# Performance work log

Measured on AMD Instinct MI355X. Metric: run time of the kernel, lower is better.

Reference implementation:

```python
import jax, jax.numpy as jnp
import numpy as np

NUM_SLOTS = 8
SLOT_DIM = 64
HIDDEN_DIM = 128  # max(slot_dim, 128)
ITERS = 3
EPS = 1e-08
LN_EPS = 1e-05


def _ln(x, w, b):
    mu = jnp.mean(x, axis=-1, keepdims=True)
    var = jnp.mean(jnp.square(x - mu), axis=-1, keepdims=True)
    return (x - mu) * jax.lax.rsqrt(var + LN_EPS) * w + b


def setup_inputs() -> dict:
    key = jax.random.key(0)
    ks = jax.random.split(key, 16)
    b, n, d, h, n_s = 64, 4096, SLOT_DIM, HIDDEN_DIM, NUM_SLOTS
    s = 1.0 / np.sqrt(d)
    sh = 1.0 / np.sqrt(h)
    inp = {
        'inputs': jax.random.normal(ks[0], (b, n, d), jnp.float32),
        'mask': jax.random.randint(ks[1], (b, n), 0, 2, jnp.int32),
        'noise': jax.random.normal(ks[2], (b, n_s, d), jnp.float32),
        'slots_mu': jax.random.normal(ks[3], (1, 1, d), jnp.float32),
        'slots_sigma': jax.random.uniform(ks[4], (1, 1, d), jnp.float32),
        'Wq': jax.random.normal(ks[5], (d, d), jnp.float32) * s,
        'bq': jnp.zeros((d,), jnp.float32),
        'Wk': jax.random.normal(ks[6], (d, d), jnp.float32) * s,
        'bk': jnp.zeros((d,), jnp.float32),
        'Wv': jax.random.normal(ks[7], (d, d), jnp.float32) * s,
        'bv': jnp.zeros((d,), jnp.float32),
        'W_ih': jax.random.normal(ks[8], (3 * d, d), jnp.float32) * s,
        'b_ih': jnp.zeros((3 * d,), jnp.float32),
        'W_hh': jax.random.normal(ks[9], (3 * d, d), jnp.float32) * s,
        'b_hh': jnp.zeros((3 * d,), jnp.float32),
        'W1': jax.random.normal(ks[10], (h, d), jnp.float32) * s,
        'b1': jnp.zeros((h,), jnp.float32),
        'W2': jax.random.normal(ks[11], (d, h), jnp.float32) * sh,
        'b2': jnp.zeros((d,), jnp.float32),
        'ln_in_w': jnp.ones((d,), jnp.float32), 'ln_in_b': jnp.zeros((d,), jnp.float32),
        'ln_s_w': jnp.ones((d,), jnp.float32), 'ln_s_b': jnp.zeros((d,), jnp.float32),
        'ln_ff_w': jnp.ones((d,), jnp.float32), 'ln_ff_b': jnp.zeros((d,), jnp.float32),
    }
    return inp


def reference(inputs, mask, noise, slots_mu, slots_sigma, Wq, bq, Wk, bk, Wv, bv,
              W_ih, b_ih, W_hh, b_hh, W1, b1, W2, b2,
              ln_in_w, ln_in_b, ln_s_w, ln_s_b, ln_ff_w, ln_ff_b):
    b, n, d = inputs.shape
    scale = d ** (-0.5)
    # slots ~ Normal(mu, sigma) via reparameterization with fixed noise
    slots = slots_mu + slots_sigma * noise  # [b, n_s, d]
    m = (mask[:, :, None] != 0)  # [b, n, 1]
    x = _ln(inputs, ln_in_w, ln_in_b)
    k = x @ Wk.T + bk  # [b, n, d]
    v = x @ Wv.T + bv  # [b, n, d]
    for _ in range(ITERS):
        slots_prev = slots
        s_n = _ln(slots, ln_s_w, ln_s_b)
        q = s_n @ Wq.T + bq  # [b, n_s, d]
        dots = jnp.einsum('bid,bjd->bij', k, q) * scale  # [b, n, n_s]
        attn = jax.nn.softmax(dots, axis=-1) + EPS
        attn = jnp.where(m, attn, 0.0)
        attn = attn / jnp.sum(attn, axis=-2, keepdims=True)
        updates = jnp.einsum('bij,bid->bjd', attn, v)  # [b, n_s, d]
        # GRUCell(updates, slots_prev)
        gx = updates @ W_ih.T + b_ih  # [b, n_s, 3d]
        gh = slots_prev @ W_hh.T + b_hh
        xr, xz, xn = jnp.split(gx, 3, axis=-1)
        hr, hz, hn = jnp.split(gh, 3, axis=-1)
        r = jax.nn.sigmoid(xr + hr)
        z = jax.nn.sigmoid(xz + hz)
        nn_ = jnp.tanh(xn + r * hn)
        slots = (1.0 - z) * nn_ + z * slots_prev
        # residual MLP
        ff = _ln(slots, ln_ff_w, ln_ff_b)
        slots = slots + (jax.nn.relu(ff @ W1.T + b1) @ W2.T + b2)
    return slots
```

## Files before the change

kernel.cpp:

```cpp
#include <hip/hip_runtime.h>
#include <hip/hip_bf16.h>

typedef unsigned short u16;
typedef unsigned int u32;
typedef unsigned long long u64;

#define BB 64
#define NN 4096
#define DD 64
#define NSLOT 8
#define HH 128
#define NITER 3

#define BF16_ONES_PROBE 0x3F803F80u

#define OFF_BQ   53248
#define OFF_BK   53312
#define OFF_BV   53376
#define OFF_BIH  53440
#define OFF_BHH  53632
#define OFF_B1   53824
#define OFF_B2   53952
#define OFF_LIW  54016
#define OFF_LIB  54080
#define OFF_LSW  54144
#define OFF_LSB  54208
#define OFF_LFW  54272
#define OFF_LFB  54336
#define OFF_PK   58496

__device__ __forceinline__ float bf2f(u16 u) {
    union { u32 i; float f; } c; c.i = ((u32)u) << 16; return c.f;
}
__device__ __forceinline__ float bflo(u32 w) {
    union { u32 i; float f; } c; c.i = w << 16; return c.f;
}
__device__ __forceinline__ float bfhi(u32 w) {
    union { u32 i; float f; } c; c.i = w & 0xffff0000u; return c.f;
}
__device__ __forceinline__ u16 f2bf(float f) {
    __hip_bfloat16 h = __float2bfloat16(f);
    return *reinterpret_cast<u16*>(&h);
}
__device__ __forceinline__ float ldf(const void* p, int i, bool isbf) {
    return isbf ? bf2f(((const u16*)p)[i]) : ((const float*)p)[i];
}

__device__ __forceinline__ float wsum64(float x) {
    #pragma unroll
    for (int o = 32; o > 0; o >>= 1) x += __shfl_xor(x, o);
    return x;
}

__device__ __forceinline__ float ln64(float v, const float* __restrict__ g,
                                      const float* __restrict__ b, int lane) {
    float mu = wsum64(v) * (1.f / 64.f);
    float d = v - mu;
    float var = wsum64(d * d) * (1.f / 64.f);
    return d * rsqrtf(var + 1e-5f) * g[lane] + b[lane];
}

__device__ __forceinline__ float mat64b(const float* __restrict__ xs,
                                        const float* __restrict__ P, int lane) {
    const float4* p4 = (const float4*)P;
    const float4* x4 = (const float4*)xs;
    float a0 = 0.f, a1 = 0.f, a2 = 0.f, a3 = 0.f;
    #pragma unroll
    for (int c = 0; c < 16; c += 4) {
        float4 x0 = x4[c], x1 = x4[c + 1], x2 = x4[c + 2], x3 = x4[c + 3];
        float4 w0 = p4[c * 64 + lane];
        float4 w1 = p4[(c + 1) * 64 + lane];
        float4 w2 = p4[(c + 2) * 64 + lane];
        float4 w3 = p4[(c + 3) * 64 + lane];
        a0 += w0.x * x0.x + w0.y * x0.y + w0.z * x0.z + w0.w * x0.w;
        a1 += w1.x * x1.x + w1.y * x1.y + w1.z * x1.z + w1.w * x1.w;
        a2 += w2.x * x2.x + w2.y * x2.y + w2.z * x2.z + w2.w * x2.w;
        a3 += w3.x * x3.x + w3.y * x3.y + w3.z * x3.z + w3.w * x3.w;
    }
    return (a0 + a1) + (a2 + a3);
}

struct PrepArgs {
    const void* w[7];
    const void* v[13];
};

__global__ __launch_bounds__(256) void prep_w(PrepArgs a, float* __restrict__ wf,
                                              const u32* __restrict__ probe) {
    bool isbf = (*probe == BF16_ONES_PROBE);
    int idx = blockIdx.x * 256 + threadIdx.x;
    if (idx < 13 * 4096) {
        int blk = idx >> 12, r = idx & 4095;
        int c = r >> 8, rem = r & 255, j = rem >> 2, dd = rem & 3;
        int m = 4 * c + dd;
        float val;
        if      (blk == 0)  val = ldf(a.w[2], j * 64 + m, isbf);
        else if (blk == 1)  val = ldf(a.w[0], j * 64 + m, isbf);
        else if (blk == 2)  val = ldf(a.w[1], m * 64 + j, isbf);
        else if (blk < 6)   val = ldf(a.w[3], ((blk - 3) * 64 + j) * 64 + m, isbf);
        else if (blk < 9)   val = ldf(a.w[4], ((blk - 6) * 64 + j) * 64 + m, isbf);
        else if (blk < 11)  val = ldf(a.w[5], ((blk - 9) * 64 + j) * 64 + m, isbf);
        else                val = ldf(a.w[6], j * 128 + (blk - 11) * 64 + m, isbf);
        wf[OFF_PK + idx] = val;
    } else {
        int k = idx - 13 * 4096;
        const int voff[13] = {OFF_BQ, OFF_BK, OFF_BV, OFF_BIH, OFF_BHH, OFF_B1, OFF_B2,
                              OFF_LIW, OFF_LIB, OFF_LSW, OFF_LSB, OFF_LFW, OFF_LFB};
        const int vn[13]   = {64, 64, 64, 192, 192, 128, 64, 64, 64, 64, 64, 64, 64};
        #pragma unroll
        for (int t = 0; t < 13; t++) {
            if (k < vn[t]) { wf[voff[t] + k] = ldf(a.v[t], k, isbf); return; }
            k -= vn[t];
        }
    }
}

__device__ __forceinline__ void emit_qstate(
        float qv, int b, int s, int bs, int lane, const float* __restrict__ wf,
        float* __restrict__ xa,
        float* __restrict__ gqp, float* __restrict__ Avec, float* __restrict__ Cvec) {
    __syncthreads();
    xa[lane] = qv;
    __syncthreads();
    float qkv = mat64b(xa, wf + OFF_PK + 2 * 4096, lane);
    float g_in = wf[OFF_LIW + lane];
    float b_in = wf[OFF_LIB + lane];
    float gqv = g_in * qkv;
    gqp[(b << 9) + (lane >> 2) * 32 + s * 4 + (lane & 3)] = gqv;
    float A  = wsum64(gqv);
    float bd = wsum64(qv * wf[OFF_BK + lane]);
    float cq = wsum64(b_in * qkv);
    if (lane == 0) { Avec[bs] = A; Cvec[bs] = cq + bd; }
}

__global__ __launch_bounds__(64, 1) void init_slots(
        const void* __restrict__ noise, const void* __restrict__ mu, const void* __restrict__ sg,
        const float* __restrict__ wf, float* __restrict__ slots,
        float* __restrict__ gqp, float* __restrict__ Avec, float* __restrict__ Cvec,
        float* __restrict__ acc1, float* __restrict__ ssv, float* __restrict__ A2v,
        const u32* __restrict__ probe) {
    __shared__ __align__(16) float xa[64];
    bool isbf = (*probe == BF16_ONES_PROBE);
    int bs = blockIdx.x;
    int b = bs >> 3, s = bs & 7;
    int i = threadIdx.x;
    int idx = bs * DD + i;
    float sl = ldf(mu, i, isbf) + ldf(sg, i, isbf) * ldf(noise, idx, isbf);
    slots[idx] = sl;
    acc1[idx] = 0.f;
    if (i == 0) { ssv[bs] = 0.f; A2v[bs] = 0.f; }
    float sn = ln64(sl, wf + OFF_LSW, wf + OFF_LSB, i);
    xa[i] = sn;
    __syncthreads();
    float qv = wf[OFF_BQ + i] + mat64b(xa, wf + OFF_PK + 1 * 4096, i);
    emit_qstate(qv, b, s, bs, i, wf, xa, gqp, Avec, Cvec);
}

#define PROC4(xv, c) do {                                                         \
    sum += xv.x + xv.y + xv.z + xv.w;                                             \
    sq  += xv.x * xv.x + xv.y * xv.y + xv.z * xv.z + xv.w * xv.w;                 \
    _Pragma("unroll")                                                             \
    for (int s = 0; s < 8; s++) {                                                 \
        float4 q = gq_s[(c) * 8 + s];                                             \
        d[s] += q.x * xv.x + q.y * xv.y + q.z * xv.z + q.w * xv.w;                \
    } } while (0)

__global__ __launch_bounds__(256) void fused_attn(
        const void* __restrict__ xin, const int* __restrict__ mask,
        const float* __restrict__ gqp, const float* __restrict__ Avec,
        const float* __restrict__ Cvec,
        float* __restrict__ acc1, float* __restrict__ ssv, float* __restrict__ A2v,
        const u32* __restrict__ probe) {
    __shared__ float4 gq_s[128];
    __shared__ float4 aw4[256][2];
    __shared__ float racc[4][NSLOT][64];
    __shared__ float rss[4][NSLOT];
    __shared__ float rA2[4][NSLOT];
    __shared__ u64 wmask[4];

    bool isbf = (*probe == BF16_ONES_PROBE);
    int b = blockIdx.x >> 4;
    int base = (blockIdx.x & 15) << 8;
    int tid = threadIdx.x;
    int wave = tid >> 6, lane = tid & 63;

    if (tid < 128) gq_s[tid] = ((const float4*)(gqp + ((size_t)b << 9)))[tid];

    size_t gt = ((size_t)b << 12) + base + tid;
    int mk = mask[gt];
    uint4 xrg[8];
    if (mk && isbf) {
        const uint4* xr = (const uint4*)((const u16*)xin + gt * 64);
        #pragma unroll
        for (int i = 0; i < 8; i++) xrg[i] = xr[i];
    }
    __syncthreads();

    float sum = 0.f, sq = 0.f;
    float d[8] = {0.f, 0.f, 0.f, 0.f, 0.f, 0.f, 0.f, 0.f};
    if (mk) {
        if (isbf) {
            #pragma unroll
            for (int c = 0; c < 16; c++) {
                u32 wa = (c & 1) ? xrg[c >> 1].z : xrg[c >> 1].x;
                u32 wb = (c & 1) ? xrg[c >> 1].w : xrg[c >> 1].y;
                float4 xv;
                xv.x = bflo(wa); xv.y = bfhi(wa); xv.z = bflo(wb); xv.w = bfhi(wb);
                PROC4(xv, c);
            }
        } else {
            const float4* xr = (const float4*)((const float*)xin + gt * 64);
            #pragma unroll
            for (int cc = 0; cc < 4; cc++) {
                float4 x0 = xr[4 * cc], x1 = xr[4 * cc + 1];
                float4 x2 = xr[4 * cc + 2], x3 = xr[4 * cc + 3];
                PROC4(x0, 4 * cc + 0);
                PROC4(x1, 4 * cc + 1);
                PROC4(x2, 4 * cc + 2);
                PROC4(x3, 4 * cc + 3);
            }
        }
    }
    float muv = sum * (1.f / 64.f);
    float var = sq * (1.f / 64.f) - muv * muv;
    float rs = rsqrtf(var + 1e-5f);
    const float* Av = Avec + (b << 3);
    const float* Cv = Cvec + (b << 3);
    #pragma unroll
    for (int s = 0; s < 8; s++)
        d[s] = 0.125f * (rs * d[s] - rs * muv * Av[s] + Cv[s]);

    float mx = d[0];
    #pragma unroll
    for (int s = 1; s < 8; s++) mx = fmaxf(mx, d[s]);
    float den = 0.f;
    #pragma unroll
    for (int s = 0; s < 8; s++) { d[s] = expf(d[s] - mx); den += d[s]; }
    float inv = 1.f / den;
    float attn[8], aw[8];
    #pragma unroll
    for (int s = 0; s < 8; s++) {
        attn[s] = (mk != 0) ? (d[s] * inv + 1e-8f) : 0.f;
        aw[s] = attn[s] * rs;
    }
    {
        float4 w0; w0.x = aw[0]; w0.y = aw[1]; w0.z = aw[2]; w0.w = aw[3];
        float4 w1; w1.x = aw[4]; w1.y = aw[5]; w1.z = aw[6]; w1.w = aw[7];
        aw4[tid][0] = w0;
        aw4[tid][1] = w1;
    }
    u64 bal = __ballot(mk != 0);
    if (lane == 0) wmask[wave] = bal;
    #pragma unroll
    for (int s = 0; s < 8; s++) {
        float t1 = wsum64(attn[s]);
        float t2 = wsum64(aw[s] * muv);
        if (lane == 0) { rss[wave][s] = t1; rA2[wave][s] = t2; }
    }
    __syncthreads();

    u64 bits = wmask[wave];
    float acc[8] = {0.f, 0.f, 0.f, 0.f, 0.f, 0.f, 0.f, 0.f};
    size_t rowbase = ((size_t)b << 12) + base + (wave << 6);
    const u16* xb16 = (const u16*)xin + rowbase * 64 + lane;
    const float* xf32 = (const float*)xin + rowbase * 64 + lane;
    #pragma unroll 8
    for (int t = 0; t < 64; t++) {
        if ((bits >> t) & 1ULL) {
            float xv = isbf ? bf2f(xb16[t * 64]) : xf32[t * 64];
            float4 a0 = aw4[(wave << 6) + t][0];
            float4 a1 = aw4[(wave << 6) + t][1];
            acc[0] += a0.x * xv; acc[1] += a0.y * xv; acc[2] += a0.z * xv; acc[3] += a0.w * xv;
            acc[4] += a1.x * xv; acc[5] += a1.y * xv; acc[6] += a1.z * xv; acc[7] += a1.w * xv;
        }
    }
    #pragma unroll
    for (int s = 0; s < 8; s++) racc[wave][s][lane] = acc[s];
    __syncthreads();
    if (wave == 0) {
        float* ag = acc1 + ((size_t)b << 9);
        #pragma unroll
        for (int s = 0; s < 8; s++) {
            float v = racc[0][s][lane] + racc[1][s][lane] + racc[2][s][lane] + racc[3][s][lane];
            atomicAdd(ag + s * 64 + lane, v);
        }
        if (lane < NSLOT) {
            float t1 = rss[0][lane] + rss[1][lane] + rss[2][lane] + rss[3][lane];
            float t2 = rA2[0][lane] + rA2[1][lane] + rA2[2][lane] + rA2[3][lane];
            atomicAdd(ssv + (b << 3) + lane, t1);
            atomicAdd(A2v + (b << 3) + lane, t2);
        }
    }
}

__global__ __launch_bounds__(64, 1) void finalize_k(
        const float* __restrict__ wf, float* __restrict__ acc1, float* __restrict__ ssv,
        float* __restrict__ A2v, float* __restrict__ slots,
        float* __restrict__ gqp, float* __restrict__ Avec, float* __restrict__ Cvec,
        void* __restrict__ out, int last, const u32* __restrict__ probe) {
    __shared__ __align__(16) float xa[64];
    __shared__ __align__(16) float xb[64];
    bool isbf = (*probe == BF16_ONES_PROBE);
    int bs = blockIdx.x;
    int b = bs >> 3, s = bs & 7;
    int i = threadIdx.x;
    int idx = bs * DD + i;
    const float* P = wf + OFF_PK;

    float sm = ssv[bs];
    float a2v_ = A2v[bs];
    float ac = acc1[idx];
    acc1[idx] = 0.f;
    if (i == 0) { ssv[bs] = 0.f; A2v[bs] = 0.f; }

    float un = wf[OFF_LIW + i] * (ac - a2v_) / sm + wf[OFF_LIB + i];

    xa[i] = un;
    __syncthreads();
    float uv = wf[OFF_BV + i] + mat64b(xa, P + 0 * 4096, i);
    float sp = slots[idx];
    __syncthreads();
    xa[i] = uv; xb[i] = sp;
    __syncthreads();

    const float4* x4a = (const float4*)xa;
    const float4* x4b = (const float4*)xb;
    const float4* pxr = (const float4*)(P + 3 * 4096);
    const float4* pxz = (const float4*)(P + 4 * 4096);
    const float4* pxn = (const float4*)(P + 5 * 4096);
    const float4* phr = (const float4*)(P + 6 * 4096);
    const float4* phz = (const float4*)(P + 7 * 4096);
    const float4* phn = (const float4*)(P + 8 * 4096);
    float xr0 = 0.f, xr1 = 0.f, xz0 = 0.f, xz1 = 0.f, xn0 = 0.f, xn1 = 0.f;
    float hr0 = 0.f, hr1 = 0.f, hz0 = 0.f, hz1 = 0.f, hn0 = 0.f, hn1 = 0.f;
    #pragma unroll
    for (int c = 0; c < 16; c += 2) {
        float4 u0 = x4a[c], u1 = x4a[c + 1];
        float4 p0 = x4b[c], p1 = x4b[c + 1];
        float4 a;
        a = pxr[c * 64 + i];       xr0 += a.x * u0.x + a.y * u0.y + a.z * u0.z + a.w * u0.w;
        a = pxr[(c + 1) * 64 + i]; xr1 += a.x * u1.x + a.y * u1.y + a.z * u1.z + a.w * u1.w;
        a = pxz[c * 64 + i];       xz0 += a.x * u0.x + a.y * u0.y + a.z * u0.z + a.w * u0.w;
        a = pxz[(c + 1) * 64 + i]; xz1 += a.x * u1.x + a.y * u1.y + a.z * u1.z + a.w * u1.w;
        a = pxn[c * 64 + i];       xn0 += a.x * u0.x + a.y * u0.y + a.z * u0.z + a.w * u0.w;
        a = pxn[(c + 1) * 64 + i]; xn1 += a.x * u1.x + a.y * u1.y + a.z * u1.z + a.w * u1.w;
        a = phr[c * 64 + i];       hr0 += a.x * p0.x + a.y * p0.y + a.z * p0.z + a.w * p0.w;
        a = phr[(c + 1) * 64 + i]; hr1 += a.x * p1.x + a.y * p1.y + a.z * p1.z + a.w * p1.w;
        a = phz[c * 64 + i];       hz0 += a.x * p0.x + a.y * p0.y + a.z * p0.z + a.w * p0.w;
        a = phz[(c + 1) * 64 + i]; hz1 += a.x * p1.x + a.y * p1.y + a.z * p1.z + a.w * p1.w;
        a = phn[c * 64 + i];       hn0 += a.x * p0.x + a.y * p0.y + a.z * p0.z + a.w * p0.w;
        a = phn[(c + 1) * 64 + i]; hn1 += a.x * p1.x + a.y * p1.y + a.z * p1.z + a.w * p1.w;
    }
    float r = 1.f / (1.f + expf(-(wf[OFF_BIH + i] + xr0 + xr1 + wf[OFF_BHH + i] + hr0 + hr1)));
    float z = 1.f / (1.f + expf(-(wf[OFF_BIH + 64 + i] + xz0 + xz1 + wf[OFF_BHH + 64 + i] + hz0 + hz1)));
    float nn = tanhf(wf[OFF_BIH + 128 + i] + xn0 + xn1 + r * (wf[OFF_BHH + 128 + i] + hn0 + hn1));
    float snew = (1.f - z) * nn + z * sp;

    float ff = ln64(snew, wf + OFF_LFW, wf + OFF_LFB, i);
    __syncthreads();
    xa[i] = ff;
    __syncthreads();
    float h1a = wf[OFF_B1 + i] + mat64b(xa, P + 9 * 4096, i);
    float h1b = wf[OFF_B1 + 64 + i] + mat64b(xa, P + 10 * 4096, i);
    h1a = fmaxf(h1a, 0.f);
    h1b = fmaxf(h1b, 0.f);
    __syncthreads();
    xa[i] = h1a; xb[i] = h1b;
    __syncthreads();
    float o = snew + wf[OFF_B2 + i] + mat64b(xa, P + 11 * 4096, i)
                                    + mat64b(xb, P + 12 * 4096, i);

    slots[idx] = o;
    if (last) {
        if (isbf) ((u16*)out)[idx] = f2bf(o);
        else      ((float*)out)[idx] = o;
    } else {
        float sn2 = ln64(o, wf + OFF_LSW, wf + OFF_LSB, i);
        __syncthreads();
        xa[i] = sn2;
        __syncthreads();
        float qv = wf[OFF_BQ + i] + mat64b(xa, P + 1 * 4096, i);
        emit_qstate(qv, b, s, bs, i, wf, xa, gqp, Avec, Cvec);
    }
}

extern "C" void kernel_launch(void* const* d_in, const int* in_sizes, int n_in,
                              void* d_out, int out_size, void* d_ws, size_t ws_size,
                              hipStream_t stream) {
    const void* xin   = d_in[0];
    const int* mask   = (const int*)d_in[1];
    const void* noise = d_in[2];
    const void* mu    = d_in[3];
    const void* sg    = d_in[4];
    const u32* probe  = (const u32*)d_in[19];

    char* ws = (char*)d_ws;
    float* wf = (float*)ws;

    size_t o = 524288;
    float* gqp   = (float*)(ws + o); o += (size_t)BB * 512 * 4;
    float* Avec  = (float*)(ws + o); o += (size_t)BB * NSLOT * 4;
    float* Cvec  = (float*)(ws + o); o += (size_t)BB * NSLOT * 4;
    float* acc1  = (float*)(ws + o); o += (size_t)BB * NSLOT * DD * 4;
    float* ssv   = (float*)(ws + o); o += (size_t)BB * NSLOT * 4;
    float* A2v   = (float*)(ws + o); o += (size_t)BB * NSLOT * 4;
    float* slots = (float*)(ws + o); o += (size_t)BB * NSLOT * DD * 4;

    PrepArgs pa;
    pa.w[0] = d_in[5];
    pa.w[1] = d_in[7];
    pa.w[2] = d_in[9];
    pa.w[3] = d_in[11];
    pa.w[4] = d_in[13];
    pa.w[5] = d_in[15];
    pa.w[6] = d_in[17];
    static const int vidx[13] = {6, 8, 10, 12, 14, 16, 18, 19, 20, 21, 22, 23, 24};
    for (int j = 0; j < 13; j++) pa.v[j] = d_in[vidx[j]];

    prep_w<<<213, 256, 0, stream>>>(pa, wf, probe);
    init_slots<<<BB * NSLOT, 64, 0, stream>>>(noise, mu, sg, wf, slots,
                                              gqp, Avec, Cvec, acc1, ssv, A2v, probe);

    for (int it = 0; it < NITER; it++) {
        fused_attn<<<BB * 16, 256, 0, stream>>>(xin, mask, gqp, Avec, Cvec,
                                                acc1, ssv, A2v, probe);
        finalize_k<<<BB * NSLOT, 64, 0, stream>>>(wf, acc1, ssv, A2v, slots,
                                                  gqp, Avec, Cvec,
                                                  d_out, it == NITER - 1 ? 1 : 0, probe);
    }
}
```

Before: 272.7 us.

## Split small slot matvecs across four waves and read query state from global memory

The per-slot init and finalize kernels go from one wave to four. Each wave computes a quarter of the K dimension of every 64x64 matvec, and the partial sums are reduced through shared memory. This is meant to shorten the serial latency of the GRU/MLP chain in these latency-bound small kernels, at the cost of more barriers. Separately, fused_attn drops its shared-memory staging of the query vectors and its initial barrier, reading them directly from global or L1 instead. It also now loads and computes on masked-out tokens unconditionally, which removes divergence but adds loads and math for every token.

```diff
diff --git a/kernel.cpp b/kernel.cpp
--- a/kernel.cpp
+++ b/kernel.cpp
@@ -60,23 +60,21 @@
     return d * rsqrtf(var + 1e-5f) * g[lane] + b[lane];
 }
 
-__device__ __forceinline__ float mat64b(const float* __restrict__ xs,
-                                        const float* __restrict__ P, int lane) {
+__device__ __forceinline__ float mat64q(const float* __restrict__ xs,
+                                        const float* __restrict__ P,
+                                        int lane, int wq) {
     const float4* p4 = (const float4*)P;
     const float4* x4 = (const float4*)xs;
-    float a0 = 0.f, a1 = 0.f, a2 = 0.f, a3 = 0.f;
-    #pragma unroll
-    for (int c = 0; c < 16; c += 4) {
-        float4 x0 = x4[c], x1 = x4[c + 1], x2 = x4[c + 2], x3 = x4[c + 3];
-        float4 w0 = p4[c * 64 + lane];
-        float4 w1 = p4[(c + 1) * 64 + lane];
-        float4 w2 = p4[(c + 2) * 64 + lane];
-        float4 w3 = p4[(c + 3) * 64 + lane];
-        a0 += w0.x * x0.x + w0.y * x0.y + w0.z * x0.z + w0.w * x0.w;
-        a1 += w1.x * x1.x + w1.y * x1.y + w1.z * x1.z + w1.w * x1.w;
-        a2 += w2.x * x2.x + w2.y * x2.y + w2.z * x2.z + w2.w * x2.w;
-        a3 += w3.x * x3.x + w3.y * x3.y + w3.z * x3.z + w3.w * x3.w;
-    }
+    int c0 = wq << 2;
+    float4 x0 = x4[c0], x1 = x4[c0 + 1], x2 = x4[c0 + 2], x3 = x4[c0 + 3];
+    float4 w0 = p4[c0 * 64 + lane];
+    float4 w1 = p4[(c0 + 1) * 64 + lane];
+    float4 w2 = p4[(c0 + 2) * 64 + lane];
+    float4 w3 = p4[(c0 + 3) * 64 + lane];
+    float a0 = w0.x * x0.x + w0.y * x0.y + w0.z * x0.z + w0.w * x0.w;
+    float a1 = w1.x * x1.x + w1.y * x1.y + w1.z * x1.z + w1.w * x1.w;
+    float a2 = w2.x * x2.x + w2.y * x2.y + w2.z * x2.z + w2.w * x2.w;
+    float a3 = w3.x * x3.x + w3.y * x3.y + w3.z * x3.z + w3.w * x3.w;
     return (a0 + a1) + (a2 + a3);
 }
 
@@ -115,55 +113,51 @@
     }
 }
 
-__device__ __forceinline__ void emit_qstate(
-        float qv, int b, int s, int bs, int lane, const float* __restrict__ wf,
-        float* __restrict__ xa,
+__device__ __forceinline__ void emit_qstate4(
+        float qv, int b, int s, int bs, int lane, int wave,
+        const float* __restrict__ wf, float* __restrict__ xa,
+        float (*__restrict__ red)[64],
         float* __restrict__ gqp, float* __restrict__ Avec, float* __restrict__ Cvec) {
-    __syncthreads();
-    xa[lane] = qv;
-    __syncthreads();
-    float qkv = mat64b(xa, wf + OFF_PK + 2 * 4096, lane);
-    float g_in = wf[OFF_LIW + lane];
-    float b_in = wf[OFF_LIB + lane];
-    float gqv = g_in * qkv;
-    gqp[(b << 9) + (lane >> 2) * 32 + s * 4 + (lane & 3)] = gqv;
+    if (wave == 0) xa[lane] = qv;
+    __syncthreads();
+    red[wave][lane] = mat64q(xa, wf + OFF_PK + 2 * 4096, lane, wave);
+    __syncthreads();
+    float qkv = red[0][lane] + red[1][lane] + red[2][lane] + red[3][lane];
+    float gqv = wf[OFF_LIW + lane] * qkv;
+    if (wave == 0) gqp[(b << 9) + (lane >> 2) * 32 + s * 4 + (lane & 3)] = gqv;
     float A  = wsum64(gqv);
     float bd = wsum64(qv * wf[OFF_BK + lane]);
-    float cq = wsum64(b_in * qkv);
-    if (lane == 0) { Avec[bs] = A; Cvec[bs] = cq + bd; }
-}
-
-__global__ __launch_bounds__(64, 1) void init_slots(
+    float cq = wsum64(wf[OFF_LIB + lane] * qkv);
+    if (wave == 0 && lane == 0) { Avec[bs] = A; Cvec[bs] = cq + bd; }
+}
+
+__global__ __launch_bounds__(256, 1) void init_slots(
         const void* __restrict__ noise, const void* __restrict__ mu, const void* __restrict__ sg,
         const float* __restrict__ wf, float* __restrict__ slots,
         float* __restrict__ gqp, float* __restrict__ Avec, float* __restrict__ Cvec,
         float* __restrict__ acc1, float* __restrict__ ssv, float* __restrict__ A2v,
         const u32* __restrict__ probe) {
     __shared__ __align__(16) float xa[64];
+    __shared__ float red[4][64];
     bool isbf = (*probe == BF16_ONES_PROBE);
     int bs = blockIdx.x;
     int b = bs >> 3, s = bs & 7;
-    int i = threadIdx.x;
-    int idx = bs * DD + i;
-    float sl = ldf(mu, i, isbf) + ldf(sg, i, isbf) * ldf(noise, idx, isbf);
-    slots[idx] = sl;
-    acc1[idx] = 0.f;
-    if (i == 0) { ssv[bs] = 0.f; A2v[bs] = 0.f; }
-    float sn = ln64(sl, wf + OFF_LSW, wf + OFF_LSB, i);
-    xa[i] = sn;
-    __syncthreads();
-    float qv = wf[OFF_BQ + i] + mat64b(xa, wf + OFF_PK + 1 * 4096, i);
-    emit_qstate(qv, b, s, bs, i, wf, xa, gqp, Avec, Cvec);
-}
-
-#define PROC4(xv, c) do {                                                         \
-    sum += xv.x + xv.y + xv.z + xv.w;                                             \
-    sq  += xv.x * xv.x + xv.y * xv.y + xv.z * xv.z + xv.w * xv.w;                 \
-    _Pragma("unroll")                                                             \
-    for (int s = 0; s < 8; s++) {                                                 \
-        float4 q = gq_s[(c) * 8 + s];                                             \
-        d[s] += q.x * xv.x + q.y * xv.y + q.z * xv.z + q.w * xv.w;                \
-    } } while (0)
+    int tid = threadIdx.x, wave = tid >> 6, lane = tid & 63;
+    int idx = bs * DD + lane;
+    float sl = ldf(mu, lane, isbf) + ldf(sg, lane, isbf) * ldf(noise, idx, isbf);
+    if (wave == 0) {
+        slots[idx] = sl;
+        acc1[idx] = 0.f;
+        if (lane == 0) { ssv[bs] = 0.f; A2v[bs] = 0.f; }
+    }
+    float sn = ln64(sl, wf + OFF_LSW, wf + OFF_LSB, lane);
+    if (wave == 0) xa[lane] = sn;
+    __syncthreads();
+    red[wave][lane] = mat64q(xa, wf + OFF_PK + 1 * 4096, lane, wave);
+    __syncthreads();
+    float qv = wf[OFF_BQ + lane] + red[0][lane] + red[1][lane] + red[2][lane] + red[3][lane];
+    emit_qstate4(qv, b, s, bs, lane, wave, wf, xa, red, gqp, Avec, Cvec);
+}
 
 __global__ __launch_bounds__(256) void fused_attn(
         const void* __restrict__ xin, const int* __restrict__ mask,
@@ -171,7 +165,6 @@
         const float* __restrict__ Cvec,
         float* __restrict__ acc1, float* __restrict__ ssv, float* __restrict__ A2v,
         const u32* __restrict__ probe) {
-    __shared__ float4 gq_s[128];
     __shared__ float4 aw4[256][2];
     __shared__ float racc[4][NSLOT][64];
     __shared__ float rss[4][NSLOT];
@@ -184,40 +177,40 @@
     int tid = threadIdx.x;
     int wave = tid >> 6, lane = tid & 63;
 
-    if (tid < 128) gq_s[tid] = ((const float4*)(gqp + ((size_t)b << 9)))[tid];
-
     size_t gt = ((size_t)b << 12) + base + tid;
     int mk = mask[gt];
-    uint4 xrg[8];
-    if (mk && isbf) {
+    const float4* gq4 = (const float4*)(gqp + ((size_t)b << 9));
+    float sum = 0.f, sq = 0.f;
+    float d[8] = {0.f, 0.f, 0.f, 0.f, 0.f, 0.f, 0.f, 0.f};
+    if (isbf) {
         const uint4* xr = (const uint4*)((const u16*)xin + gt * 64);
+        uint4 xrg[8];
         #pragma unroll
         for (int i = 0; i < 8; i++) xrg[i] = xr[i];
-    }
-    __syncthreads();
-
-    float sum = 0.f, sq = 0.f;
-    float d[8] = {0.f, 0.f, 0.f, 0.f, 0.f, 0.f, 0.f, 0.f};
-    if (mk) {
-        if (isbf) {
+        #pragma unroll
+        for (int c = 0; c < 16; c++) {
+            u32 wa = (c & 1) ? xrg[c >> 1].z : xrg[c >> 1].x;
+            u32 wb = (c & 1) ? xrg[c >> 1].w : xrg[c >> 1].y;
+            float x0 = bflo(wa), x1 = bfhi(wa), x2 = bflo(wb), x3 = bfhi(wb);
+            sum += x0 + x1 + x2 + x3;
+            sq  += x0 * x0 + x1 * x1 + x2 * x2 + x3 * x3;
             #pragma unroll
-            for (int c = 0; c < 16; c++) {
-                u32 wa = (c & 1) ? xrg[c >> 1].z : xrg[c >> 1].x;
-                u32 wb = (c & 1) ? xrg[c >> 1].w : xrg[c >> 1].y;
-                float4 xv;
-                xv.x = bflo(wa); xv.y = bfhi(wa); xv.z = bflo(wb); xv.w = bfhi(wb);
-                PROC4(xv, c);
+            for (int s = 0; s < 8; s++) {
+                float4 q = gq4[c * 8 + s];
+                d[s] += q.x * x0 + q.y * x1 + q.z * x2 + q.w * x3;
             }
-        } else {
-            const float4* xr = (const float4*)((const float*)xin + gt * 64);
+        }
+    } else {
+        const float4* xr = (const float4*)((const float*)xin + gt * 64);
+        #pragma unroll
+        for (int c = 0; c < 16; c++) {
+            float4 xv = xr[c];
+            sum += xv.x + xv.y + xv.z + xv.w;
+            sq  += xv.x * xv.x + xv.y * xv.y + xv.z * xv.z + xv.w * xv.w;
             #pragma unroll
-            for (int cc = 0; cc < 4; cc++) {
-                float4 x0 = xr[4 * cc], x1 = xr[4 * cc + 1];
-                float4 x2 = xr[4 * cc + 2], x3 = xr[4 * cc + 3];
-                PROC4(x0, 4 * cc + 0);
-                PROC4(x1, 4 * cc + 1);
-                PROC4(x2, 4 * cc + 2);
-                PROC4(x3, 4 * cc + 3);
+            for (int s = 0; s < 8; s++) {
+                float4 q = gq4[c * 8 + s];
+                d[s] += q.x * xv.x + q.y * xv.y + q.z * xv.z + q.w * xv.w;
             }
         }
     }
@@ -246,8 +239,7 @@
     {
         float4 w0; w0.x = aw[0]; w0.y = aw[1]; w0.z = aw[2]; w0.w = aw[3];
         float4 w1; w1.x = aw[4]; w1.y = aw[5]; w1.z = aw[6]; w1.w = aw[7];
-        aw4[tid][0] = w0;
-        aw4[tid][1] = w1;
+        aw4[tid][0] = w0; aw4[tid][1] = w1;
     }
     u64 bal = __ballot(mk != 0);
     if (lane == 0) wmask[wave] = bal;
@@ -270,8 +262,10 @@
             float xv = isbf ? bf2f(xb16[t * 64]) : xf32[t * 64];
             float4 a0 = aw4[(wave << 6) + t][0];
             float4 a1 = aw4[(wave << 6) + t][1];
-            acc[0] += a0.x * xv; acc[1] += a0.y * xv; acc[2] += a0.z * xv; acc[3] += a0.w * xv;
-            acc[4] += a1.x * xv; acc[5] += a1.y * xv; acc[6] += a1.z * xv; acc[7] += a1.w * xv;
+            acc[0] += a0.x * xv; acc[1] += a0.y * xv;
+            acc[2] += a0.z * xv; acc[3] += a0.w * xv;
+            acc[4] += a1.x * xv; acc[5] += a1.y * xv;
+            acc[6] += a1.z * xv; acc[7] += a1.w * xv;
         }
     }
     #pragma unroll
@@ -293,95 +287,90 @@
     }
 }
 
-__global__ __launch_bounds__(64, 1) void finalize_k(
+__global__ __launch_bounds__(256, 1) void finalize_k(
         const float* __restrict__ wf, float* __restrict__ acc1, float* __restrict__ ssv,
         float* __restrict__ A2v, float* __restrict__ slots,
         float* __restrict__ gqp, float* __restrict__ Avec, float* __restrict__ Cvec,
         void* __restrict__ out, int last, const u32* __restrict__ probe) {
     __shared__ __align__(16) float xa[64];
     __shared__ __align__(16) float xb[64];
+    __shared__ float red[6][4][64];
     bool isbf = (*probe == BF16_ONES_PROBE);
     int bs = blockIdx.x;
     int b = bs >> 3, s = bs & 7;
-    int i = threadIdx.x;
-    int idx = bs * DD + i;
+    int tid = threadIdx.x, wave = tid >> 6, lane = tid & 63;
+    int idx = bs * DD + lane;
     const float* P = wf + OFF_PK;
 
-    float sm = ssv[bs];
+    float sm   = ssv[bs];
     float a2v_ = A2v[bs];
-    float ac = acc1[idx];
-    acc1[idx] = 0.f;
-    if (i == 0) { ssv[bs] = 0.f; A2v[bs] = 0.f; }
-
-    float un = wf[OFF_LIW + i] * (ac - a2v_) / sm + wf[OFF_LIB + i];
-
-    xa[i] = un;
-    __syncthreads();
-    float uv = wf[OFF_BV + i] + mat64b(xa, P + 0 * 4096, i);
-    float sp = slots[idx];
-    __syncthreads();
-    xa[i] = uv; xb[i] = sp;
-    __syncthreads();
-
-    const float4* x4a = (const float4*)xa;
-    const float4* x4b = (const float4*)xb;
-    const float4* pxr = (const float4*)(P + 3 * 4096);
-    const float4* pxz = (const float4*)(P + 4 * 4096);
-    const float4* pxn = (const float4*)(P + 5 * 4096);
-    const float4* phr = (const float4*)(P + 6 * 4096);
-    const float4* phz = (const float4*)(P + 7 * 4096);
-    const float4* phn = (const float4*)(P + 8 * 4096);
-    float xr0 = 0.f, xr1 = 0.f, xz0 = 0.f, xz1 = 0.f, xn0 = 0.f, xn1 = 0.f;
-    float hr0 = 0.f, hr1 = 0.f, hz0 = 0.f, hz1 = 0.f, hn0 = 0.f, hn1 = 0.f;
-    #pragma unroll
-    for (int c = 0; c < 16; c += 2) {
-        float4 u0 = x4a[c], u1 = x4a[c + 1];
-        float4 p0 = x4b[c], p1 = x4b[c + 1];
-        float4 a;
-        a = pxr[c * 64 + i];       xr0 += a.x * u0.x + a.y * u0.y + a.z * u0.z + a.w * u0.w;
-        a = pxr[(c + 1) * 64 + i]; xr1 += a.x * u1.x + a.y * u1.y + a.z * u1.z + a.w * u1.w;
-        a = pxz[c * 64 + i];       xz0 += a.x * u0.x + a.y * u0.y + a.z * u0.z + a.w * u0.w;
-        a = pxz[(c + 1) * 64 + i]; xz1 += a.x * u1.x + a.y * u1.y + a.z * u1.z + a.w * u1.w;
-        a = pxn[c * 64 + i];       xn0 += a.x * u0.x + a.y * u0.y + a.z * u0.z + a.w * u0.w;
-        a = pxn[(c + 1) * 64 + i]; xn1 += a.x * u1.x + a.y * u1.y + a.z * u1.z + a.w * u1.w;
-        a = phr[c * 64 + i];       hr0 += a.x * p0.x + a.y * p0.y + a.z * p0.z + a.w * p0.w;
-        a = phr[(c + 1) * 64 + i]; hr1 += a.x * p1.x + a.y * p1.y + a.z * p1.z + a.w * p1.w;
-        a = phz[c * 64 + i];       hz0 += a.x * p0.x + a.y * p0.y + a.z * p0.z + a.w * p0.w;
-        a = phz[(c + 1) * 64 + i]; hz1 += a.x * p1.x + a.y * p1.y + a.z * p1.z + a.w * p1.w;
-        a = phn[c * 64 + i];       hn0 += a.x * p0.x + a.y * p0.y + a.z * p0.z + a.w * p0.w;
-        a = phn[(c + 1) * 64 + i]; hn1 += a.x * p1.x + a.y * p1.y + a.z * p1.z + a.w * p1.w;
-    }
-    float r = 1.f / (1.f + expf(-(wf[OFF_BIH + i] + xr0 + xr1 + wf[OFF_BHH + i] + hr0 + hr1)));
-    float z = 1.f / (1.f + expf(-(wf[OFF_BIH + 64 + i] + xz0 + xz1 + wf[OFF_BHH + 64 + i] + hz0 + hz1)));
-    float nn = tanhf(wf[OFF_BIH + 128 + i] + xn0 + xn1 + r * (wf[OFF_BHH + 128 + i] + hn0 + hn1));
+    float ac   = acc1[idx];
+    float sp   = slots[idx];
+
+    float un = wf[OFF_LIW + lane] * (ac - a2v_) / sm + wf[OFF_LIB + lane];
+    if (wave == 0) xa[lane] = un;
+    __syncthreads();
+    if (wave == 0) {
+        acc1[idx] = 0.f;
+        if (lane == 0) { ssv[bs] = 0.f; A2v[bs] = 0.f; }
+    }
+
+    red[0][wave][lane] = mat64q(xa, P + 0 * 4096, lane, wave);
+    __syncthreads();
+    #define SUM4(k) (red[k][0][lane] + red[k][1][lane] + red[k][2][lane] + red[k][3][lane])
+    float uv = wf[OFF_BV + lane] + SUM4(0);
+    if (wave == 0) { xa[lane] = uv; xb[lane] = sp; }
+    __syncthreads();
+
+    red[0][wave][lane] = mat64q(xa, P + 3 * 4096, lane, wave);
+    red[1][wave][lane] = mat64q(xa, P + 4 * 4096, lane, wave);
+    red[2][wave][lane] = mat64q(xa, P + 5 * 4096, lane, wave);
+    red[3][wave][lane] = mat64q(xb, P + 6 * 4096, lane, wave);
+    red[4][wave][lane] = mat64q(xb, P + 7 * 4096, lane, wave);
+    red[5][wave][lane] = mat64q(xb, P + 8 * 4096, lane, wave);
+    __syncthreads();
+    float gxr = wf[OFF_BIH + lane]       + SUM4(0);
+    float gxz = wf[OFF_BIH + 64 + lane]  + SUM4(1);
+    float gxn = wf[OFF_BIH + 128 + lane] + SUM4(2);
+    float ghr = wf[OFF_BHH + lane]       + SUM4(3);
+    float ghz = wf[OFF_BHH + 64 + lane]  + SUM4(4);
+    float ghn = wf[OFF_BHH + 128 + lane] + SUM4(5);
+    float r = 1.f / (1.f + expf(-(gxr + ghr)));
+    float z = 1.f / (1.f + expf(-(gxz + ghz)));
+    float nn = tanhf(gxn + r * ghn);
     float snew = (1.f - z) * nn + z * sp;
 
-    float ff = ln64(snew, wf + OFF_LFW, wf + OFF_LFB, i);
-    __syncthreads();
-    xa[i] = ff;
-    __syncthreads();
-    float h1a = wf[OFF_B1 + i] + mat64b(xa, P + 9 * 4096, i);
-    float h1b = wf[OFF_B1 + 64 + i] + mat64b(xa, P + 10 * 4096, i);
-    h1a = fmaxf(h1a, 0.f);
-    h1b = fmaxf(h1b, 0.f);
-    __syncthreads();
-    xa[i] = h1a; xb[i] = h1b;
-    __syncthreads();
-    float o = snew + wf[OFF_B2 + i] + mat64b(xa, P + 11 * 4096, i)
-                                    + mat64b(xb, P + 12 * 4096, i);
-
-    slots[idx] = o;
+    float ff = ln64(snew, wf + OFF_LFW, wf + OFF_LFB, lane);
+    if (wave == 0) xa[lane] = ff;
+    __syncthreads();
+    red[0][wave][lane] = mat64q(xa, P + 9 * 4096, lane, wave);
+    red[1][wave][lane] = mat64q(xa, P + 10 * 4096, lane, wave);
+    __syncthreads();
+    float h1a = fmaxf(wf[OFF_B1 + lane] + SUM4(0), 0.f);
+    float h1b = fmaxf(wf[OFF_B1 + 64 + lane] + SUM4(1), 0.f);
+    if (wave == 0) { xa[lane] = h1a; xb[lane] = h1b; }
+    __syncthreads();
+    red[0][wave][lane] = mat64q(xa, P + 11 * 4096, lane, wave)
+                       + mat64q(xb, P + 12 * 4096, lane, wave);
+    __syncthreads();
+    float o = snew + wf[OFF_B2 + lane] + SUM4(0);
+
+    if (wave == 0) slots[idx] = o;
     if (last) {
-        if (isbf) ((u16*)out)[idx] = f2bf(o);
-        else      ((float*)out)[idx] = o;
+        if (wave == 0) {
+            if (isbf) ((u16*)out)[idx] = f2bf(o);
+            else      ((float*)out)[idx] = o;
+        }
     } else {
-        float sn2 = ln64(o, wf + OFF_LSW, wf + OFF_LSB, i);
+        float sn2 = ln64(o, wf + OFF_LSW, wf + OFF_LSB, lane);
+        if (wave == 0) xa[lane] = sn2;
         __syncthreads();
-        xa[i] = sn2;
+        red[0][wave][lane] = mat64q(xa, P + 1 * 4096, lane, wave);
         __syncthreads();
-        float qv = wf[OFF_BQ + i] + mat64b(xa, P + 1 * 4096, i);
-        emit_qstate(qv, b, s, bs, i, wf, xa, gqp, Avec, Cvec);
-    }
+        float qv = wf[OFF_BQ + lane] + SUM4(0);
+        emit_qstate4(qv, b, s, bs, lane, wave, wf, xa, red[0], gqp, Avec, Cvec);
+    }
+    #undef SUM4
 }
 
 extern "C" void kernel_launch(void* const* d_in, const int* in_sizes, int n_in,
@@ -418,14 +407,14 @@
     for (int j = 0; j < 13; j++) pa.v[j] = d_in[vidx[j]];
 
     prep_w<<<213, 256, 0, stream>>>(pa, wf, probe);
-    init_slots<<<BB * NSLOT, 64, 0, stream>>>(noise, mu, sg, wf, slots,
-                                              gqp, Avec, Cvec, acc1, ssv, A2v, probe);
+    init_slots<<<BB * NSLOT, 256, 0, stream>>>(noise, mu, sg, wf, slots,
+                                               gqp, Avec, Cvec, acc1, ssv, A2v, probe);
 
     for (int it = 0; it < NITER; it++) {
         fused_attn<<<BB * 16, 256, 0, stream>>>(xin, mask, gqp, Avec, Cvec,
                                                 acc1, ssv, A2v, probe);
-        finalize_k<<<BB * NSLOT, 64, 0, stream>>>(wf, acc1, ssv, A2v, slots,
-                                                  gqp, Avec, Cvec,
-                                                  d_out, it == NITER - 1 ? 1 : 0, probe);
-    }
-}
+        finalize_k<<<BB * NSLOT, 256, 0, stream>>>(wf, acc1, ssv, A2v, slots,
+                                                   gqp, Avec, Cvec,
+                                                   d_out, it == NITER - 1 ? 1 : 0, probe);
+    }
+}
```

After: 291.3 us. 6.8% more time.
